# Kernel optimization log

Measured on AMD Instinct MI355X. Metric: run time of the kernel, lower is better.

## Reference

```python
import jax, jax.numpy as jnp
import numpy as np

EPS = 1e-10
N_USER, N_ITEM, D = 100000, 50000, 64
E_R, E_T = 500000, 250000


def setup_inputs() -> dict:
    key = jax.random.key(0)
    ks = jax.random.split(key, 32)
    f32 = jnp.float32
    inp = {
        'x_u': jax.random.normal(ks[0], (N_USER, D), f32),
        'x_i': jax.random.normal(ks[1], (N_ITEM, D), f32),
        'a_u': jax.random.normal(ks[2], (N_USER, D), f32),
        'a_i': jax.random.normal(ks[3], (N_ITEM, D), f32),
        't': jax.random.normal(ks[4], (N_USER, D), f32),
        'boun3': jax.random.uniform(ks[5], (E_R,), f32),
        'user_intent': 0.01 * jax.random.uniform(ks[6], (N_USER, D), f32),
        'item_intent': 0.01 * jax.random.uniform(ks[7], (N_ITEM, D), f32),
        'W_att_w': jax.random.normal(ks[8], (2 * D, 1), f32) * 0.05,
        'W_att_b': jax.random.normal(ks[9], (1,), f32) * 0.05,
        'W4_w': jax.random.normal(ks[10], (4 * D, 2 * D), f32) * 0.05,
        'W4_b': jax.random.normal(ks[11], (2 * D,), f32) * 0.05,
        'W5_w': jax.random.normal(ks[12], (2 * D, D), f32) * 0.05,
        'W5_b': jax.random.normal(ks[13], (D,), f32) * 0.05,
        'W6_w': jax.random.normal(ks[14], (D, 1), f32) * 0.05,
        'W6_b': jax.random.normal(ks[15], (1,), f32) * 0.05,
        'W_so_w': jax.random.normal(ks[16], (2 * D, D), f32) * 0.05,
        'W_so_b': jax.random.normal(ks[17], (D,), f32) * 0.05,
        'W_so2_w': jax.random.normal(ks[18], (D, 1), f32) * 0.05,
        'W_so2_b': jax.random.normal(ks[19], (1,), f32) * 0.05,
        'rated_src': jax.random.randint(ks[20], (E_R,), 0, N_USER, jnp.int32),
        'rated_dst': jax.random.randint(ks[21], (E_R,), 0, N_ITEM, jnp.int32),
        'tp_src': jax.random.randint(ks[22], (E_T,), 0, N_USER, jnp.int32),
        'tp_dst': jax.random.randint(ks[23], (E_T,), 0, N_USER, jnp.int32),
        'tn_src': jax.random.randint(ks[24], (E_T,), 0, N_USER, jnp.int32),
        'tn_dst': jax.random.randint(ks[25], (E_T,), 0, N_USER, jnp.int32),
    }
    return inp


def _trust_score(t, src, dst, W_so_w, W_so_b, W_so2_w, W_so2_b):
    # solinkpre: sigmoid(W_so2(W_so(cat(t_src, t_dst)))) per edge  -> [E]
    h = jnp.concatenate([t[src], t[dst]], axis=1)          # [E, 2D]
    h = h @ W_so_w + W_so_b                                # [E, D] (no activation, as in source)
    return jax.nn.sigmoid(h @ W_so2_w + W_so2_b)[:, 0]


def _rmse(label, pred):
    dis = label - pred + EPS
    return jnp.sqrt(jnp.sum(dis * dis) / pred.shape[0])


def reference(x_u, x_i, a_u, a_i, t, boun3, user_intent, item_intent,
              W_att_w, W_att_b, W4_w, W4_b, W5_w, W5_b, W6_w, W6_b,
              W_so_w, W_so_b, W_so2_w, W_so2_b,
              rated_src, rated_dst, tp_src, tp_dst, tn_src, tn_dst):
    n_item = x_i.shape[0]
    # simple_ls + fn.max reduce: per-edge rowwise dot (torch.diag(mm) -> vectorized),
    # segment-max onto dst item nodes
    sim_ls = jax.nn.sigmoid(jnp.sum(user_intent[rated_src] * x_i[rated_dst], axis=-1))  # [E_R]
    a_sim = jax.ops.segment_max(sim_ls, rated_dst, num_segments=n_item)                 # [n_item]
    # attitude: sigmoid(W_att(cat(a_src, a_dst)))
    att = jax.nn.sigmoid(
        jnp.concatenate([a_u[rated_src], a_i[rated_dst]], axis=1) @ W_att_w + W_att_b
    )[:, 0]                                                                             # [E_R]
    # linear_s: a_sim[dst] * where(att>=0.5, 0, -0)  (identically zero, kept faithful)
    score = a_sim[rated_dst] * jnp.where(att >= 0.5, 0.0, -0.0)
    # _add_influ_mlp_concat: W6(W5(W4(cat(item_intent[dst], x_src, x_dst, user_intent[src]))))
    h = jnp.concatenate(
        [item_intent[rated_dst], x_u[rated_src], x_i[rated_dst], user_intent[rated_src]], axis=1
    )                                                                                   # [E_R, 4D]
    influ = (((h @ W4_w + W4_b) @ W5_w + W5_b) @ W6_w + W6_b)[:, 0]
    pos_score = score + influ
    # attitude RMSE against boun3 labels
    l_att = _rmse(boun3, att)
    # trust link prediction on pos and neg graphs
    pos_t = _trust_score(t, tp_src, tp_dst, W_so_w, W_so_b, W_so2_w, W_so2_b)
    neg_t = _trust_score(t, tn_src, tn_dst, W_so_w, W_so_b, W_so2_w, W_so2_b)
    score_t = jnp.concatenate([pos_t, neg_t])
    label = jnp.concatenate([jnp.ones_like(pos_t), jnp.zeros_like(neg_t)])
    loss_trust = _rmse(label, score_t)
    # roc_auc / average_precision (jnp equivalents of sklearn metrics)
    n = score_t.shape[0]
    P = jnp.sum(label)
    N = n - P
    order = jnp.argsort(score_t)
    ranks = jnp.zeros(n, score_t.dtype).at[order].set(jnp.arange(1, n + 1, dtype=score_t.dtype))
    auc = (jnp.sum(ranks * label) - P * (P + 1) / 2) / (P * N)
    desc = jnp.argsort(-score_t)
    l_sorted = label[desc]
    prec = jnp.cumsum(l_sorted) / jnp.arange(1, n + 1, dtype=score_t.dtype)
    ap = jnp.sum(prec * l_sorted) / P
    return pos_score, l_att, auc, ap, loss_trust
```

## Files before the change

kernel.cpp:

```cpp
#include <hip/hip_runtime.h>

#define N_USER 100000
#define N_ITEM 50000
#define E_R    500000
#define E_T    250000
#define NB     (1 << 20)
#define NCH    4096
#define ZMIN   (-4.0f)
#define ZSCALE ((float)NB / 8.0f)
#define NBLK_R 512
#define NBLK_T 512

__device__ __forceinline__ float sigmoidf(float z) {
  return 1.0f / (1.0f + expf(-z));
}

__device__ __forceinline__ float dot4(float4 a, float4 b) {
  return a.x * b.x + a.y * b.y + a.z * b.z + a.w * b.w;
}

__device__ __forceinline__ float wave_sum_f(float v) {
#pragma unroll
  for (int off = 32; off > 0; off >>= 1) v += __shfl_xor(v, off, 64);
  return v;
}

__device__ __forceinline__ double wave_sum_d(double v) {
#pragma unroll
  for (int off = 32; off > 0; off >>= 1) v += __shfl_xor(v, off, 64);
  return v;
}

__global__ void k_collapse(const float* __restrict__ W4w, const float* __restrict__ W4b,
                           const float* __restrict__ W5w, const float* __restrict__ W5b,
                           const float* __restrict__ W6w, const float* __restrict__ W6b,
                           const float* __restrict__ Wsow, const float* __restrict__ Wsob,
                           const float* __restrict__ Wso2w, const float* __restrict__ Wso2b,
                           float* __restrict__ wts) {
  __shared__ float v56[128];
  int t = threadIdx.x;
  if (t < 128) {
    float s = 0.f;
    for (int k = 0; k < 64; ++k) s += W5w[t * 64 + k] * W6w[k];
    v56[t] = s;
  }
  __syncthreads();
  {
    float s = 0.f;
    for (int j = 0; j < 128; ++j) s += W4w[t * 128 + j] * v56[j];
    wts[t] = s;
  }
  if (t < 128) {
    float s = 0.f;
    for (int k = 0; k < 64; ++k) s += Wsow[t * 64 + k] * Wso2w[k];
    wts[320 + t] = s;
  }
  if (t < 64) {
    float pb = W5b[t] * W6w[t] + W4b[t] * v56[t] + W4b[64 + t] * v56[64 + t];
    float ps = Wsob[t] * Wso2w[t];
    pb = wave_sum_f(pb);
    ps = wave_sum_f(ps);
    if (t == 0) {
      wts[256] = pb + W6b[0];
      wts[448] = ps + Wso2b[0];
    }
  }
}

__global__ void k_nodes(const float* __restrict__ xu, const float* __restrict__ ui,
                        const float* __restrict__ au, const float* __restrict__ tt,
                        const float* __restrict__ xi, const float* __restrict__ ii,
                        const float* __restrict__ ai,
                        const float* __restrict__ Wattw, const float* __restrict__ wts,
                        float2* __restrict__ u_rate, float2* __restrict__ u_trust,
                        float2* __restrict__ i_rate) {
  int lane = threadIdx.x & 63;
  int wib = threadIdx.x >> 6;
  int g = lane >> 4;
  int q = lane & 15;
  if (blockIdx.x < 1024) {
    const float4* xu4 = (const float4*)xu;
    const float4* ui4 = (const float4*)ui;
    const float4* au4 = (const float4*)au;
    const float4* tt4 = (const float4*)tt;
    float4 wex = ((const float4*)(wts + 64))[q];
    float4 weu = ((const float4*)(wts + 192))[q];
    float4 wa  = ((const float4*)Wattw)[q];
    float4 w1  = ((const float4*)(wts + 320))[q];
    float4 w2  = ((const float4*)(wts + 384))[q];
    int wave = blockIdx.x * 4 + wib;
    const int nw = 4096;
    for (int tile = wave; tile < N_USER / 4; tile += nw) {
      int node = tile * 4 + g;
      int base = node * 16 + q;
      float4 x = xu4[base], uv = ui4[base], a = au4[base], tv = tt4[base];
      float s0 = dot4(x, wex) + dot4(uv, weu);
      float s1 = dot4(a, wa);
      float s2 = dot4(tv, w1);
      float s3 = dot4(tv, w2);
#pragma unroll
      for (int off = 1; off < 16; off <<= 1) {
        s0 += __shfl_xor(s0, off, 64);
        s1 += __shfl_xor(s1, off, 64);
        s2 += __shfl_xor(s2, off, 64);
        s3 += __shfl_xor(s3, off, 64);
      }
      if (q == 0) {
        u_rate[node]  = make_float2(s0, s1);
        u_trust[node] = make_float2(s2, s3);
      }
    }
  } else {
    const float4* xi4 = (const float4*)xi;
    const float4* ii4 = (const float4*)ii;
    const float4* ai4 = (const float4*)ai;
    float4 wei  = ((const float4*)(wts + 0))[q];
    float4 wexi = ((const float4*)(wts + 128))[q];
    float4 wai  = ((const float4*)(Wattw + 64))[q];
    int wave = (blockIdx.x - 1024) * 4 + wib;
    const int nw = 2048;
    for (int tile = wave; tile < N_ITEM / 4; tile += nw) {
      int node = tile * 4 + g;
      int base = node * 16 + q;
      float4 x = xi4[base], iv = ii4[base], a = ai4[base];
      float s0 = dot4(iv, wei) + dot4(x, wexi);
      float s1 = dot4(a, wai);
#pragma unroll
      for (int off = 1; off < 16; off <<= 1) {
        s0 += __shfl_xor(s0, off, 64);
        s1 += __shfl_xor(s1, off, 64);
      }
      if (q == 0) i_rate[node] = make_float2(s0, s1);
    }
  }
}

__global__ void k_edges(const int* __restrict__ src, const int* __restrict__ dst,
                        const float* __restrict__ boun3,
                        const float2* __restrict__ u_rate, const float2* __restrict__ i_rate,
                        const int* __restrict__ tps, const int* __restrict__ tpd,
                        const int* __restrict__ tns, const int* __restrict__ tnd,
                        const float2* __restrict__ u_trust,
                        const float* __restrict__ wts, const float* __restrict__ Wattb,
                        float* __restrict__ out,
                        unsigned* __restrict__ histP, unsigned* __restrict__ histN,
                        double* __restrict__ partR, double* __restrict__ partT) {
  __shared__ double sd[4];
  float local = 0.f;
  if (blockIdx.x < NBLK_R) {
    float batt = Wattb[0];
    float beff = wts[256];
    const int4* src4 = (const int4*)src;
    const int4* dst4 = (const int4*)dst;
    const float4* b4 = (const float4*)boun3;
    float4* out4 = (float4*)out;
    for (int e = blockIdx.x * 256 + threadIdx.x; e < E_R / 4; e += NBLK_R * 256) {
      int4 s = src4[e], d = dst4[e];
      float4 bo = b4[e];
      float2 ur0 = u_rate[s.x], ur1 = u_rate[s.y], ur2 = u_rate[s.z], ur3 = u_rate[s.w];
      float2 ir0 = i_rate[d.x], ir1 = i_rate[d.y], ir2 = i_rate[d.z], ir3 = i_rate[d.w];
      out4[e] = make_float4(ur0.x + ir0.x + beff, ur1.x + ir1.x + beff,
                            ur2.x + ir2.x + beff, ur3.x + ir3.x + beff);
      float d0 = bo.x - sigmoidf(ur0.y + ir0.y + batt) + 1e-10f;
      float d1 = bo.y - sigmoidf(ur1.y + ir1.y + batt) + 1e-10f;
      float d2 = bo.z - sigmoidf(ur2.y + ir2.y + batt) + 1e-10f;
      float d3 = bo.w - sigmoidf(ur3.y + ir3.y + batt) + 1e-10f;
      local += d0 * d0 + d1 * d1 + d2 * d2 + d3 * d3;
    }
    float w = wave_sum_f(local);
    if ((threadIdx.x & 63) == 0) sd[threadIdx.x >> 6] = (double)w;
    __syncthreads();
    if (threadIdx.x == 0) partR[blockIdx.x] = sd[0] + sd[1] + sd[2] + sd[3];
  } else {
    float bso = wts[448];
    int b = blockIdx.x - NBLK_R;
    const int4* tps4 = (const int4*)tps;
    const int4* tpd4 = (const int4*)tpd;
    const int4* tns4 = (const int4*)tns;
    const int4* tnd4 = (const int4*)tnd;
    for (int e = b * 256 + threadIdx.x; e < 2 * E_T / 4; e += NBLK_T * 256) {
      int4 s, d;
      int lab;
      if (e < E_T / 4) { s = tps4[e]; d = tpd4[e]; lab = 1; }
      else             { s = tns4[e - E_T / 4]; d = tnd4[e - E_T / 4]; lab = 0; }
      unsigned* hist = lab ? histP : histN;
      float z0 = u_trust[s.x].x + u_trust[d.x].y + bso;
      float z1 = u_trust[s.y].x + u_trust[d.y].y + bso;
      float z2 = u_trust[s.z].x + u_trust[d.z].y + bso;
      float z3 = u_trust[s.w].x + u_trust[d.w].y + bso;
      float base = lab ? 1.0f : 0.0f;
      float d0 = base - sigmoidf(z0) + 1e-10f;
      float d1 = base - sigmoidf(z1) + 1e-10f;
      float d2 = base - sigmoidf(z2) + 1e-10f;
      float d3 = base - sigmoidf(z3) + 1e-10f;
      local += d0 * d0 + d1 * d1 + d2 * d2 + d3 * d3;
      int b0 = (int)((z0 - ZMIN) * ZSCALE); b0 = b0 < 0 ? 0 : (b0 >= NB ? NB - 1 : b0);
      int b1 = (int)((z1 - ZMIN) * ZSCALE); b1 = b1 < 0 ? 0 : (b1 >= NB ? NB - 1 : b1);
      int b2 = (int)((z2 - ZMIN) * ZSCALE); b2 = b2 < 0 ? 0 : (b2 >= NB ? NB - 1 : b2);
      int b3 = (int)((z3 - ZMIN) * ZSCALE); b3 = b3 < 0 ? 0 : (b3 >= NB ? NB - 1 : b3);
      atomicAdd(&hist[b0], 1u);
      atomicAdd(&hist[b1], 1u);
      atomicAdd(&hist[b2], 1u);
      atomicAdd(&hist[b3], 1u);
    }
    float w = wave_sum_f(local);
    if ((threadIdx.x & 63) == 0) sd[threadIdx.x >> 6] = (double)w;
    __syncthreads();
    if (threadIdx.x == 0) partT[b] = sd[0] + sd[1] + sd[2] + sd[3];
  }
}

__global__ void k_chunksum(const uint4* __restrict__ hP4, const uint4* __restrict__ hN4,
                           unsigned* __restrict__ chP, unsigned* __restrict__ chN) {
  int t = threadIdx.x, lane = t & 63, w = t >> 6;
  int chunk = blockIdx.x * 4 + w;
  int idx = chunk * 64 + lane;
  uint4 p = hP4[idx], n = hN4[idx];
  unsigned sp = p.x + p.y + p.z + p.w;
  unsigned sn = n.x + n.y + n.z + n.w;
#pragma unroll
  for (int off = 32; off > 0; off >>= 1) {
    sp += __shfl_xor(sp, off, 64);
    sn += __shfl_xor(sn, off, 64);
  }
  if (lane == 0) { chP[chunk] = sp; chN[chunk] = sn; }
}

__global__ void k_scan(const unsigned* __restrict__ chP, const unsigned* __restrict__ chN,
                       unsigned* __restrict__ prefP, unsigned* __restrict__ prefN) {
  __shared__ unsigned shp[1024], shn[1024];
  int t = threadIdx.x;
  int base = t * 4;
  unsigned ep[4], en[4], runp = 0, runn = 0;
#pragma unroll
  for (int i = 0; i < 4; ++i) {
    ep[i] = runp; en[i] = runn;
    runp += chP[base + i]; runn += chN[base + i];
  }
  shp[t] = runp; shn[t] = runn;
  __syncthreads();
  for (int off = 1; off < 1024; off <<= 1) {
    unsigned ap_ = 0, an_ = 0;
    if (t >= off) { ap_ = shp[t - off]; an_ = shn[t - off]; }
    __syncthreads();
    shp[t] += ap_; shn[t] += an_;
    __syncthreads();
  }
  unsigned exP = shp[t] - runp, exN = shn[t] - runn;
#pragma unroll
  for (int i = 0; i < 4; ++i) {
    prefP[base + i] = exP + ep[i];
    prefN[base + i] = exN + en[i];
  }
}

__global__ void k_aucap(const unsigned* __restrict__ histP, const unsigned* __restrict__ histN,
                        const unsigned* __restrict__ prefP, const unsigned* __restrict__ prefN,
                        double* __restrict__ partC, double* __restrict__ partA) {
  __shared__ unsigned sp[256], sn[256];
  int t = threadIdx.x;
  int bin = blockIdx.x * 256 + t;
  unsigned np = histP[bin], nn = histN[bin];
  sp[t] = np; sn[t] = nn;
  __syncthreads();
  for (int off = 1; off < 256; off <<= 1) {
    unsigned ap_ = 0, an_ = 0;
    if (t >= off) { ap_ = sp[t - off]; an_ = sn[t - off]; }
    __syncthreads();
    sp[t] += ap_; sn[t] += an_;
    __syncthreads();
  }
  unsigned PA = prefP[blockIdx.x] + sp[t] - np;
  unsigned NA = prefN[blockIdx.x] + sn[t] - nn;
  double Cc = (double)np * (double)NA + 0.5 * (double)np * (double)nn;
  double apc = 0.0;
  if (np > 0) {
    double cpa = (double)(E_T - PA - np);
    double cna = (double)(E_T - NA - nn);
    double ratio = (double)(np + nn) / (double)np;
    for (unsigned j = 1; j <= np; ++j) {
      double r = ((double)j - 0.5) * ratio + 0.5;
      apc += (cpa + (double)j) / (cpa + cna + r);
    }
  }
  double c = wave_sum_d(Cc);
  double a = wave_sum_d(apc);
  __shared__ double dc[4], da[4];
  int lane = t & 63, w = t >> 6;
  if (lane == 0) { dc[w] = c; da[w] = a; }
  __syncthreads();
  if (t == 0) {
    partC[blockIdx.x] = dc[0] + dc[1] + dc[2] + dc[3];
    partA[blockIdx.x] = da[0] + da[1] + da[2] + da[3];
  }
}

__global__ void k_final(const double* __restrict__ partR, const double* __restrict__ partT,
                        const double* __restrict__ partC, const double* __restrict__ partA,
                        float* __restrict__ out) {
  int t = threadIdx.x;
  double sR = 0, sT = 0, sC = 0, sA = 0;
  for (int i = t; i < NBLK_R; i += 256) sR += partR[i];
  for (int i = t; i < NBLK_T; i += 256) sT += partT[i];
  for (int i = t; i < 4096; i += 256) { sC += partC[i]; sA += partA[i]; }
  sR = wave_sum_d(sR); sT = wave_sum_d(sT);
  sC = wave_sum_d(sC); sA = wave_sum_d(sA);
  __shared__ double sh[4][4];
  int lane = t & 63, w = t >> 6;
  if (lane == 0) { sh[w][0] = sR; sh[w][1] = sT; sh[w][2] = sC; sh[w][3] = sA; }
  __syncthreads();
  if (t == 0) {
    double R = sh[0][0] + sh[1][0] + sh[2][0] + sh[3][0];
    double T = sh[0][1] + sh[1][1] + sh[2][1] + sh[3][1];
    double C = sh[0][2] + sh[1][2] + sh[2][2] + sh[3][2];
    double A = sh[0][3] + sh[1][3] + sh[2][3] + sh[3][3];
    out[E_R + 0] = (float)sqrt(R / (double)E_R);
    out[E_R + 1] = (float)(C / ((double)E_T * (double)E_T));
    out[E_R + 2] = (float)(A / (double)E_T);
    out[E_R + 3] = (float)sqrt(T / (double)(2 * E_T));
  }
}

extern "C" void kernel_launch(void* const* d_in, const int* in_sizes, int n_in,
                              void* d_out, int out_size, void* d_ws, size_t ws_size,
                              hipStream_t stream) {
  (void)in_sizes; (void)n_in; (void)out_size; (void)ws_size;
  const float* x_u        = (const float*)d_in[0];
  const float* x_i        = (const float*)d_in[1];
  const float* a_u        = (const float*)d_in[2];
  const float* a_i        = (const float*)d_in[3];
  const float* t          = (const float*)d_in[4];
  const float* boun3      = (const float*)d_in[5];
  const float* user_int   = (const float*)d_in[6];
  const float* item_int   = (const float*)d_in[7];
  const float* W_att_w    = (const float*)d_in[8];
  const float* W_att_b    = (const float*)d_in[9];
  const float* W4_w       = (const float*)d_in[10];
  const float* W4_b       = (const float*)d_in[11];
  const float* W5_w       = (const float*)d_in[12];
  const float* W5_b       = (const float*)d_in[13];
  const float* W6_w       = (const float*)d_in[14];
  const float* W6_b       = (const float*)d_in[15];
  const float* W_so_w     = (const float*)d_in[16];
  const float* W_so_b     = (const float*)d_in[17];
  const float* W_so2_w    = (const float*)d_in[18];
  const float* W_so2_b    = (const float*)d_in[19];
  const int*   rated_src  = (const int*)d_in[20];
  const int*   rated_dst  = (const int*)d_in[21];
  const int*   tp_src     = (const int*)d_in[22];
  const int*   tp_dst     = (const int*)d_in[23];
  const int*   tn_src     = (const int*)d_in[24];
  const int*   tn_dst     = (const int*)d_in[25];
  float* out = (float*)d_out;

  char* ws = (char*)d_ws;
  double* partR   = (double*)ws;
  double* partT   = partR + NBLK_R;
  double* partC   = partT + NBLK_T;
  double* partA   = partC + 4096;
  unsigned* histP = (unsigned*)(partA + 4096);
  unsigned* histN = histP + NB;
  unsigned* chP   = histN + NB;
  unsigned* chN   = chP + NCH;
  unsigned* prefP = chN + NCH;
  unsigned* prefN = prefP + NCH;
  float* wts      = (float*)(prefN + NCH);
  float2* u_rate  = (float2*)(wts + 512);
  float2* u_trust = u_rate + N_USER;
  float2* i_rate  = u_trust + N_USER;

  hipMemsetAsync(histP, 0, (size_t)2 * NB * sizeof(unsigned), stream);

  k_collapse<<<1, 256, 0, stream>>>(W4_w, W4_b, W5_w, W5_b, W6_w, W6_b,
                                    W_so_w, W_so_b, W_so2_w, W_so2_b, wts);
  k_nodes<<<1536, 256, 0, stream>>>(x_u, user_int, a_u, t, x_i, item_int, a_i,
                                    W_att_w, wts, u_rate, u_trust, i_rate);
  k_edges<<<NBLK_R + NBLK_T, 256, 0, stream>>>(rated_src, rated_dst, boun3, u_rate, i_rate,
                                    tp_src, tp_dst, tn_src, tn_dst, u_trust,
                                    wts, W_att_b, out, histP, histN, partR, partT);
  k_chunksum<<<1024, 256, 0, stream>>>((const uint4*)histP, (const uint4*)histN, chP, chN);
  k_scan<<<1, 1024, 0, stream>>>(chP, chN, prefP, prefN);
  k_aucap<<<NCH, 256, 0, stream>>>(histP, histN, prefP, prefN, partC, partA);
  k_final<<<1, 256, 0, stream>>>(partR, partT, partC, partA, out);
}
```

Before: 276.3 us.

## Fold histogram zeroing into node kernel, drop scan kernel, flatten edge grids

Removes the separate memset by having the node kernel zero the histogram, and removes the single-block k_scan by having each k_aucap block sum the preceding chunk totals itself and do a wave-shuffle intra-block scan instead of a shared-memory scan with many barriers. The node and edge kernels go from grid-stride loops to one-shot grids (two nodes per wave, two edges per thread) with larger launches. The aim is fewer launches and less serialized work, at the cost of redundant chunk-prefix reads in every aucap block (up to 4096 loads for the last block) and more partial sums to reduce.

Measured after the change: 264.6 us. 4.2% less time.

```diff
diff --git a/kernel.cpp b/kernel.cpp
--- a/kernel.cpp
+++ b/kernel.cpp
@@ -8,8 +8,10 @@
 #define NCH    4096
 #define ZMIN   (-4.0f)
 #define ZSCALE ((float)NB / 8.0f)
-#define NBLK_R 512
-#define NBLK_T 512
+#define UW     12500
+#define IW     6250
+#define TW     (UW + IW)
+#define NODE_BLOCKS ((TW + 3) / 4)
 
 __device__ __forceinline__ float sigmoidf(float z) {
   return 1.0f / (1.0f + expf(-z));
@@ -20,6 +22,12 @@
 }
 
 __device__ __forceinline__ float wave_sum_f(float v) {
+#pragma unroll
+  for (int off = 32; off > 0; off >>= 1) v += __shfl_xor(v, off, 64);
+  return v;
+}
+
+__device__ __forceinline__ unsigned wave_sum_u(unsigned v) {
 #pragma unroll
   for (int off = 32; off > 0; off >>= 1) v += __shfl_xor(v, off, 64);
   return v;
@@ -73,64 +81,76 @@
                         const float* __restrict__ ai,
                         const float* __restrict__ Wattw, const float* __restrict__ wts,
                         float2* __restrict__ u_rate, float2* __restrict__ u_trust,
-                        float2* __restrict__ i_rate) {
+                        float2* __restrict__ i_rate,
+                        uint2* __restrict__ hz) {
+  int idx = blockIdx.x * 256 + threadIdx.x;
+  if (idx < NB) hz[idx] = make_uint2(0u, 0u);
+
   int lane = threadIdx.x & 63;
-  int wib = threadIdx.x >> 6;
+  int wave = blockIdx.x * 4 + (threadIdx.x >> 6);
+  if (wave >= TW) return;
   int g = lane >> 4;
   int q = lane & 15;
-  if (blockIdx.x < 1024) {
+
+  if (wave < UW) {
     const float4* xu4 = (const float4*)xu;
     const float4* ui4 = (const float4*)ui;
     const float4* au4 = (const float4*)au;
     const float4* tt4 = (const float4*)tt;
+    int nA = wave * 8 + g;
+    int baseA = nA * 16 + q;
+    int baseB = baseA + 64;
+    float4 xA = xu4[baseA], xB = xu4[baseB];
+    float4 uA = ui4[baseA], uB = ui4[baseB];
+    float4 aA = au4[baseA], aB = au4[baseB];
+    float4 tA = tt4[baseA], tB = tt4[baseB];
     float4 wex = ((const float4*)(wts + 64))[q];
     float4 weu = ((const float4*)(wts + 192))[q];
     float4 wa  = ((const float4*)Wattw)[q];
     float4 w1  = ((const float4*)(wts + 320))[q];
     float4 w2  = ((const float4*)(wts + 384))[q];
-    int wave = blockIdx.x * 4 + wib;
-    const int nw = 4096;
-    for (int tile = wave; tile < N_USER / 4; tile += nw) {
-      int node = tile * 4 + g;
-      int base = node * 16 + q;
-      float4 x = xu4[base], uv = ui4[base], a = au4[base], tv = tt4[base];
-      float s0 = dot4(x, wex) + dot4(uv, weu);
-      float s1 = dot4(a, wa);
-      float s2 = dot4(tv, w1);
-      float s3 = dot4(tv, w2);
-#pragma unroll
-      for (int off = 1; off < 16; off <<= 1) {
-        s0 += __shfl_xor(s0, off, 64);
-        s1 += __shfl_xor(s1, off, 64);
-        s2 += __shfl_xor(s2, off, 64);
-        s3 += __shfl_xor(s3, off, 64);
-      }
-      if (q == 0) {
-        u_rate[node]  = make_float2(s0, s1);
-        u_trust[node] = make_float2(s2, s3);
-      }
+    float sA0 = dot4(xA, wex) + dot4(uA, weu);
+    float sB0 = dot4(xB, wex) + dot4(uB, weu);
+    float sA1 = dot4(aA, wa), sB1 = dot4(aB, wa);
+    float sA2 = dot4(tA, w1), sB2 = dot4(tB, w1);
+    float sA3 = dot4(tA, w2), sB3 = dot4(tB, w2);
+#pragma unroll
+    for (int off = 1; off < 16; off <<= 1) {
+      sA0 += __shfl_xor(sA0, off, 64); sB0 += __shfl_xor(sB0, off, 64);
+      sA1 += __shfl_xor(sA1, off, 64); sB1 += __shfl_xor(sB1, off, 64);
+      sA2 += __shfl_xor(sA2, off, 64); sB2 += __shfl_xor(sB2, off, 64);
+      sA3 += __shfl_xor(sA3, off, 64); sB3 += __shfl_xor(sB3, off, 64);
+    }
+    if (q == 0) {
+      u_rate[nA]      = make_float2(sA0, sA1);
+      u_trust[nA]     = make_float2(sA2, sA3);
+      u_rate[nA + 4]  = make_float2(sB0, sB1);
+      u_trust[nA + 4] = make_float2(sB2, sB3);
     }
   } else {
     const float4* xi4 = (const float4*)xi;
     const float4* ii4 = (const float4*)ii;
     const float4* ai4 = (const float4*)ai;
+    int nA = (wave - UW) * 8 + g;
+    int baseA = nA * 16 + q;
+    int baseB = baseA + 64;
+    float4 xA = xi4[baseA], xB = xi4[baseB];
+    float4 iA = ii4[baseA], iB = ii4[baseB];
+    float4 aA = ai4[baseA], aB = ai4[baseB];
     float4 wei  = ((const float4*)(wts + 0))[q];
     float4 wexi = ((const float4*)(wts + 128))[q];
     float4 wai  = ((const float4*)(Wattw + 64))[q];
-    int wave = (blockIdx.x - 1024) * 4 + wib;
-    const int nw = 2048;
-    for (int tile = wave; tile < N_ITEM / 4; tile += nw) {
-      int node = tile * 4 + g;
-      int base = node * 16 + q;
-      float4 x = xi4[base], iv = ii4[base], a = ai4[base];
-      float s0 = dot4(iv, wei) + dot4(x, wexi);
-      float s1 = dot4(a, wai);
-#pragma unroll
-      for (int off = 1; off < 16; off <<= 1) {
-        s0 += __shfl_xor(s0, off, 64);
-        s1 += __shfl_xor(s1, off, 64);
-      }
-      if (q == 0) i_rate[node] = make_float2(s0, s1);
+    float sA0 = dot4(iA, wei) + dot4(xA, wexi);
+    float sB0 = dot4(iB, wei) + dot4(xB, wexi);
+    float sA1 = dot4(aA, wai), sB1 = dot4(aB, wai);
+#pragma unroll
+    for (int off = 1; off < 16; off <<= 1) {
+      sA0 += __shfl_xor(sA0, off, 64); sB0 += __shfl_xor(sB0, off, 64);
+      sA1 += __shfl_xor(sA1, off, 64); sB1 += __shfl_xor(sB1, off, 64);
+    }
+    if (q == 0) {
+      i_rate[nA]     = make_float2(sA0, sA1);
+      i_rate[nA + 4] = make_float2(sB0, sB1);
     }
   }
 }
@@ -147,61 +167,44 @@
                         double* __restrict__ partR, double* __restrict__ partT) {
   __shared__ double sd[4];
   float local = 0.f;
-  if (blockIdx.x < NBLK_R) {
-    float batt = Wattb[0];
-    float beff = wts[256];
-    const int4* src4 = (const int4*)src;
-    const int4* dst4 = (const int4*)dst;
-    const float4* b4 = (const float4*)boun3;
-    float4* out4 = (float4*)out;
-    for (int e = blockIdx.x * 256 + threadIdx.x; e < E_R / 4; e += NBLK_R * 256) {
-      int4 s = src4[e], d = dst4[e];
-      float4 bo = b4[e];
-      float2 ur0 = u_rate[s.x], ur1 = u_rate[s.y], ur2 = u_rate[s.z], ur3 = u_rate[s.w];
-      float2 ir0 = i_rate[d.x], ir1 = i_rate[d.y], ir2 = i_rate[d.z], ir3 = i_rate[d.w];
-      out4[e] = make_float4(ur0.x + ir0.x + beff, ur1.x + ir1.x + beff,
-                            ur2.x + ir2.x + beff, ur3.x + ir3.x + beff);
+  if (blockIdx.x < 1024) {
+    int e = blockIdx.x * 256 + threadIdx.x;
+    if (e < E_R / 2) {
+      float batt = Wattb[0];
+      float beff = wts[256];
+      int2 s = ((const int2*)src)[e], d = ((const int2*)dst)[e];
+      float2 bo = ((const float2*)boun3)[e];
+      float2 ur0 = u_rate[s.x], ur1 = u_rate[s.y];
+      float2 ir0 = i_rate[d.x], ir1 = i_rate[d.y];
+      ((float2*)out)[e] = make_float2(ur0.x + ir0.x + beff, ur1.x + ir1.x + beff);
       float d0 = bo.x - sigmoidf(ur0.y + ir0.y + batt) + 1e-10f;
       float d1 = bo.y - sigmoidf(ur1.y + ir1.y + batt) + 1e-10f;
-      float d2 = bo.z - sigmoidf(ur2.y + ir2.y + batt) + 1e-10f;
-      float d3 = bo.w - sigmoidf(ur3.y + ir3.y + batt) + 1e-10f;
-      local += d0 * d0 + d1 * d1 + d2 * d2 + d3 * d3;
+      local = d0 * d0 + d1 * d1;
     }
     float w = wave_sum_f(local);
     if ((threadIdx.x & 63) == 0) sd[threadIdx.x >> 6] = (double)w;
     __syncthreads();
     if (threadIdx.x == 0) partR[blockIdx.x] = sd[0] + sd[1] + sd[2] + sd[3];
   } else {
-    float bso = wts[448];
-    int b = blockIdx.x - NBLK_R;
-    const int4* tps4 = (const int4*)tps;
-    const int4* tpd4 = (const int4*)tpd;
-    const int4* tns4 = (const int4*)tns;
-    const int4* tnd4 = (const int4*)tnd;
-    for (int e = b * 256 + threadIdx.x; e < 2 * E_T / 4; e += NBLK_T * 256) {
-      int4 s, d;
+    int b = blockIdx.x - 1024;
+    int e = b * 256 + threadIdx.x;
+    if (e < E_T) {
+      float bso = wts[448];
+      int2 s, d;
       int lab;
-      if (e < E_T / 4) { s = tps4[e]; d = tpd4[e]; lab = 1; }
-      else             { s = tns4[e - E_T / 4]; d = tnd4[e - E_T / 4]; lab = 0; }
+      if (e < E_T / 2) { s = ((const int2*)tps)[e]; d = ((const int2*)tpd)[e]; lab = 1; }
+      else { s = ((const int2*)tns)[e - E_T / 2]; d = ((const int2*)tnd)[e - E_T / 2]; lab = 0; }
       unsigned* hist = lab ? histP : histN;
       float z0 = u_trust[s.x].x + u_trust[d.x].y + bso;
       float z1 = u_trust[s.y].x + u_trust[d.y].y + bso;
-      float z2 = u_trust[s.z].x + u_trust[d.z].y + bso;
-      float z3 = u_trust[s.w].x + u_trust[d.w].y + bso;
       float base = lab ? 1.0f : 0.0f;
       float d0 = base - sigmoidf(z0) + 1e-10f;
       float d1 = base - sigmoidf(z1) + 1e-10f;
-      float d2 = base - sigmoidf(z2) + 1e-10f;
-      float d3 = base - sigmoidf(z3) + 1e-10f;
-      local += d0 * d0 + d1 * d1 + d2 * d2 + d3 * d3;
+      local = d0 * d0 + d1 * d1;
       int b0 = (int)((z0 - ZMIN) * ZSCALE); b0 = b0 < 0 ? 0 : (b0 >= NB ? NB - 1 : b0);
       int b1 = (int)((z1 - ZMIN) * ZSCALE); b1 = b1 < 0 ? 0 : (b1 >= NB ? NB - 1 : b1);
-      int b2 = (int)((z2 - ZMIN) * ZSCALE); b2 = b2 < 0 ? 0 : (b2 >= NB ? NB - 1 : b2);
-      int b3 = (int)((z3 - ZMIN) * ZSCALE); b3 = b3 < 0 ? 0 : (b3 >= NB ? NB - 1 : b3);
       atomicAdd(&hist[b0], 1u);
       atomicAdd(&hist[b1], 1u);
-      atomicAdd(&hist[b2], 1u);
-      atomicAdd(&hist[b3], 1u);
     }
     float w = wave_sum_f(local);
     if ((threadIdx.x & 63) == 0) sd[threadIdx.x >> 6] = (double)w;
@@ -218,60 +221,42 @@
   uint4 p = hP4[idx], n = hN4[idx];
   unsigned sp = p.x + p.y + p.z + p.w;
   unsigned sn = n.x + n.y + n.z + n.w;
-#pragma unroll
-  for (int off = 32; off > 0; off >>= 1) {
-    sp += __shfl_xor(sp, off, 64);
-    sn += __shfl_xor(sn, off, 64);
-  }
+  sp = wave_sum_u(sp);
+  sn = wave_sum_u(sn);
   if (lane == 0) { chP[chunk] = sp; chN[chunk] = sn; }
 }
 
-__global__ void k_scan(const unsigned* __restrict__ chP, const unsigned* __restrict__ chN,
-                       unsigned* __restrict__ prefP, unsigned* __restrict__ prefN) {
-  __shared__ unsigned shp[1024], shn[1024];
-  int t = threadIdx.x;
-  int base = t * 4;
-  unsigned ep[4], en[4], runp = 0, runn = 0;
-#pragma unroll
+__global__ void k_aucap(const unsigned* __restrict__ histP, const unsigned* __restrict__ histN,
+                        const unsigned* __restrict__ chP, const unsigned* __restrict__ chN,
+                        double* __restrict__ partC, double* __restrict__ partA) {
+  int t = threadIdx.x, lane = t & 63, w = t >> 6;
+  int blk = blockIdx.x;
+  unsigned bp = 0, bn = 0;
+  for (int c = t; c < blk; c += 256) { bp += chP[c]; bn += chN[c]; }
+  bp = wave_sum_u(bp);
+  bn = wave_sum_u(bn);
+  __shared__ unsigned sbp[4], sbn[4], swp[4], swn[4];
+  if (lane == 0) { sbp[w] = bp; sbn[w] = bn; }
+  int bin = blk * 256 + t;
+  unsigned np = histP[bin], nn = histN[bin];
+  unsigned ip = np, in_ = nn;
+#pragma unroll
+  for (int off = 1; off < 64; off <<= 1) {
+    int sl = lane >= off ? lane - off : lane;
+    unsigned tp = __shfl(ip, sl, 64);
+    unsigned tn = __shfl(in_, sl, 64);
+    if (lane >= off) { ip += tp; in_ += tn; }
+  }
+  if (lane == 63) { swp[w] = ip; swn[w] = in_; }
+  __syncthreads();
+  unsigned base_p = sbp[0] + sbp[1] + sbp[2] + sbp[3];
+  unsigned base_n = sbn[0] + sbn[1] + sbn[2] + sbn[3];
+  unsigned wo_p = 0, wo_n = 0;
   for (int i = 0; i < 4; ++i) {
-    ep[i] = runp; en[i] = runn;
-    runp += chP[base + i]; runn += chN[base + i];
-  }
-  shp[t] = runp; shn[t] = runn;
-  __syncthreads();
-  for (int off = 1; off < 1024; off <<= 1) {
-    unsigned ap_ = 0, an_ = 0;
-    if (t >= off) { ap_ = shp[t - off]; an_ = shn[t - off]; }
-    __syncthreads();
-    shp[t] += ap_; shn[t] += an_;
-    __syncthreads();
-  }
-  unsigned exP = shp[t] - runp, exN = shn[t] - runn;
-#pragma unroll
-  for (int i = 0; i < 4; ++i) {
-    prefP[base + i] = exP + ep[i];
-    prefN[base + i] = exN + en[i];
-  }
-}
-
-__global__ void k_aucap(const unsigned* __restrict__ histP, const unsigned* __restrict__ histN,
-                        const unsigned* __restrict__ prefP, const unsigned* __restrict__ prefN,
-                        double* __restrict__ partC, double* __restrict__ partA) {
-  __shared__ unsigned sp[256], sn[256];
-  int t = threadIdx.x;
-  int bin = blockIdx.x * 256 + t;
-  unsigned np = histP[bin], nn = histN[bin];
-  sp[t] = np; sn[t] = nn;
-  __syncthreads();
-  for (int off = 1; off < 256; off <<= 1) {
-    unsigned ap_ = 0, an_ = 0;
-    if (t >= off) { ap_ = sp[t - off]; an_ = sn[t - off]; }
-    __syncthreads();
-    sp[t] += ap_; sn[t] += an_;
-    __syncthreads();
-  }
-  unsigned PA = prefP[blockIdx.x] + sp[t] - np;
-  unsigned NA = prefN[blockIdx.x] + sn[t] - nn;
+    if (i < w) { wo_p += swp[i]; wo_n += swn[i]; }
+  }
+  unsigned PA = base_p + wo_p + ip - np;
+  unsigned NA = base_n + wo_n + in_ - nn;
   double Cc = (double)np * (double)NA + 0.5 * (double)np * (double)nn;
   double apc = 0.0;
   if (np > 0) {
@@ -286,12 +271,11 @@
   double c = wave_sum_d(Cc);
   double a = wave_sum_d(apc);
   __shared__ double dc[4], da[4];
-  int lane = t & 63, w = t >> 6;
   if (lane == 0) { dc[w] = c; da[w] = a; }
   __syncthreads();
   if (t == 0) {
-    partC[blockIdx.x] = dc[0] + dc[1] + dc[2] + dc[3];
-    partA[blockIdx.x] = da[0] + da[1] + da[2] + da[3];
+    partC[blk] = dc[0] + dc[1] + dc[2] + dc[3];
+    partA[blk] = da[0] + da[1] + da[2] + da[3];
   }
 }
 
@@ -300,8 +284,7 @@
                         float* __restrict__ out) {
   int t = threadIdx.x;
   double sR = 0, sT = 0, sC = 0, sA = 0;
-  for (int i = t; i < NBLK_R; i += 256) sR += partR[i];
-  for (int i = t; i < NBLK_T; i += 256) sT += partT[i];
+  for (int i = t; i < 1024; i += 256) { sR += partR[i]; sT += partT[i]; }
   for (int i = t; i < 4096; i += 256) { sC += partC[i]; sA += partA[i]; }
   sR = wave_sum_d(sR); sT = wave_sum_d(sT);
   sC = wave_sum_d(sC); sA = wave_sum_d(sA);
@@ -355,31 +338,27 @@
 
   char* ws = (char*)d_ws;
   double* partR   = (double*)ws;
-  double* partT   = partR + NBLK_R;
-  double* partC   = partT + NBLK_T;
+  double* partT   = partR + 1024;
+  double* partC   = partT + 1024;
   double* partA   = partC + 4096;
   unsigned* histP = (unsigned*)(partA + 4096);
   unsigned* histN = histP + NB;
   unsigned* chP   = histN + NB;
   unsigned* chN   = chP + NCH;
-  unsigned* prefP = chN + NCH;
-  unsigned* prefN = prefP + NCH;
-  float* wts      = (float*)(prefN + NCH);
+  float* wts      = (float*)(chN + NCH);
   float2* u_rate  = (float2*)(wts + 512);
   float2* u_trust = u_rate + N_USER;
   float2* i_rate  = u_trust + N_USER;
 
-  hipMemsetAsync(histP, 0, (size_t)2 * NB * sizeof(unsigned), stream);
-
   k_collapse<<<1, 256, 0, stream>>>(W4_w, W4_b, W5_w, W5_b, W6_w, W6_b,
                                     W_so_w, W_so_b, W_so2_w, W_so2_b, wts);
-  k_nodes<<<1536, 256, 0, stream>>>(x_u, user_int, a_u, t, x_i, item_int, a_i,
-                                    W_att_w, wts, u_rate, u_trust, i_rate);
-  k_edges<<<NBLK_R + NBLK_T, 256, 0, stream>>>(rated_src, rated_dst, boun3, u_rate, i_rate,
+  k_nodes<<<NODE_BLOCKS, 256, 0, stream>>>(x_u, user_int, a_u, t, x_i, item_int, a_i,
+                                           W_att_w, wts, u_rate, u_trust, i_rate,
+                                           (uint2*)histP);
+  k_edges<<<2048, 256, 0, stream>>>(rated_src, rated_dst, boun3, u_rate, i_rate,
                                     tp_src, tp_dst, tn_src, tn_dst, u_trust,
                                     wts, W_att_b, out, histP, histN, partR, partT);
   k_chunksum<<<1024, 256, 0, stream>>>((const uint4*)histP, (const uint4*)histN, chP, chN);
-  k_scan<<<1, 1024, 0, stream>>>(chP, chN, prefP, prefN);
-  k_aucap<<<NCH, 256, 0, stream>>>(histP, histN, prefP, prefN, partC, partA);
+  k_aucap<<<NCH, 256, 0, stream>>>(histP, histN, chP, chN, partC, partA);
   k_final<<<1, 256, 0, stream>>>(partR, partT, partC, partA, out);
 }
```
